# Kernel optimization log

Hardware: AMD Instinct MI355X
Metric: run time of the kernel (lower is better)

The kernel has to match this reference:

```python
import jax, jax.numpy as jnp
import numpy as np

B, S, HID, NH = 8, 1024, 1024, 16
HD = HID // NH  # 64
STR = 128
NEG = -1e10


def setup_inputs() -> dict:
    key = jax.random.key(0)
    ks = jax.random.split(key, 16)
    def lin(k, fan_in, fan_out):
        bound = 1.0 / np.sqrt(fan_in)
        kw, kb = jax.random.split(k)
        W = jax.random.uniform(kw, (fan_in, fan_out), jnp.float32, -bound, bound)
        b = jax.random.uniform(kb, (fan_out,), jnp.float32, -bound, bound)
        return W, b
    Wq, bq = lin(ks[0], HID, HID)
    Wk, bk = lin(ks[1], HID, HID)
    Wv, bv = lin(ks[2], HID, HID)
    Wsk, bsk = lin(ks[3], HID, STR)
    Wsv, bsv = lin(ks[4], HID, STR)
    Wo, bo = lin(ks[5], HID + STR, HID)
    return {
        "query": jax.random.normal(ks[6], (B, S, HID), jnp.float32),
        "key": jax.random.normal(ks[7], (B, S, HID), jnp.float32),
        "value": jax.random.normal(ks[8], (B, S, HID), jnp.float32),
        "x_rsa": jax.random.normal(ks[9], (B, S, STR), jnp.float32),
        "mask": jax.random.randint(ks[10], (B, 1, 1, S), 0, 2, jnp.int32),
        "rsa_mask": jax.random.randint(ks[11], (B, 1, 1, S), 0, 2, jnp.int32),
        "Wq": Wq, "bq": bq, "Wk": Wk, "bk": bk, "Wv": Wv, "bv": bv,
        "Wsk": Wsk, "bsk": bsk, "Wsv": Wsv, "bsv": bsv, "Wo": Wo, "bo": bo,
    }


def reference(query, key, value, x_rsa, mask, rsa_mask,
              Wq, bq, Wk, bk, Wv, bv, Wsk, bsk, Wsv, bsv, Wo, bo):
    scale = jnp.sqrt(jnp.float32(HD))
    Q = (query @ Wq + bq).reshape(B, S, NH, HD).transpose(0, 2, 1, 3)   # [B,NH,S,HD]
    K = (key @ Wk + bk).reshape(B, S, NH, HD).transpose(0, 2, 1, 3)
    V = (value @ Wv + bv).reshape(B, S, NH, HD).transpose(0, 2, 1, 3)
    str_K = (key @ Wsk + bsk)[:, None, :, :]    # [B,1,S,128]
    str_V = (value @ Wsv + bsv)[:, None, :, :]
    rsa_Q = x_rsa[:, None, :, :]                # [B,1,S,128]

    energy = jnp.einsum('bhqd,bhkd->bhqk', Q, K)           # [B,NH,S,S]
    rsa_energy = jnp.einsum('bhqd,bhkd->bhqk', rsa_Q, str_K)  # [B,1,S,S]
    # torch order: mask first, then divide by scale
    energy = jnp.where(mask == 0, NEG, energy) / scale
    rsa_energy = jnp.where(mask == 0, NEG, rsa_energy)
    rsa_energy = jnp.where(rsa_mask == 0, NEG, rsa_energy)  # str_scale == 1

    attention = jax.nn.softmax(energy, axis=-1)
    rsa_attention = jax.nn.softmax(rsa_energy, axis=-1)
    # dropout is identity in eval mode
    x = jnp.einsum('bhqk,bhkd->bhqd', attention, V)          # [B,NH,S,HD]
    rsa_x = jnp.einsum('bhqk,bhkd->bhqd', rsa_attention, str_V)  # [B,1,S,128]
    x = x.transpose(0, 2, 1, 3).reshape(B, S, HID)
    rsa_x = rsa_x.transpose(0, 2, 1, 3).reshape(B, S, STR)
    out = jnp.concatenate((x, rsa_x), axis=-1) @ Wo + bo     # [B,S,HID]
    return out, attention, rsa_attention
```

## Files before the change

kernel.cpp:

```cpp
#include <hip/hip_runtime.h>
#include <stdint.h>

typedef unsigned int u32;
typedef _Float16 f16_t;

typedef _Float16 f16x8 __attribute__((ext_vector_type(8)));
typedef __fp16   fp16x2 __attribute__((ext_vector_type(2)));
typedef float    f32x4 __attribute__((ext_vector_type(4)));

__device__ __forceinline__ f32x4 mfma16(f16x8 a, f16x8 b, f32x4 c){
  return __builtin_amdgcn_mfma_f32_16x16x32_f16(a, b, c, 0, 0, 0);
}
__device__ __forceinline__ float fexp2(float x){ return __builtin_amdgcn_exp2f(x); }
__device__ __forceinline__ u32 pkrtz(float a, float b){
  union { fp16x2 h; u32 u; } cv; cv.h = __builtin_amdgcn_cvt_pkrtz(a, b); return cv.u;
}

template<int N>
__device__ __forceinline__ void barrier_vmleave(){
  asm volatile("s_waitcnt vmcnt(%0)" :: "i"(N) : "memory");
  __builtin_amdgcn_s_barrier();
}

__device__ __forceinline__ void gl_lds16(const void* g, void* l){
  typedef const __attribute__((address_space(1))) void* gasp;
  typedef __attribute__((address_space(3))) void* lasp;
  gasp gp = reinterpret_cast<gasp>(reinterpret_cast<uintptr_t>(g));
  lasp lp = reinterpret_cast<lasp>(static_cast<u32>(reinterpret_cast<uintptr_t>(l)));
  __builtin_amdgcn_global_load_lds(gp, lp, 16, 0, 0);
}

template<int NBYTES, int ROWB, int NT>
__device__ __forceinline__ void stage_swz(const char* gbase, u32 gstrideB, char* lds, int tid){
  const u32 lane = (u32)(tid & 63);
  #pragma unroll
  for (int j = 0; j < NBYTES/(NT*16); ++j){
    u32 o   = (u32)(j*NT + tid) * 16u;
    u32 row = o / (u32)ROWB;
    u32 col = (o % (u32)ROWB) ^ ((row & ((u32)(ROWB>>4)-1u)) << 4);
    gl_lds16(gbase + (size_t)row * gstrideB + col, lds + (o - lane*16u));
  }
}

template<int ROWB>
__device__ __forceinline__ u32 swzb(u32 row, u32 col){
  return col ^ ((row & ((u32)(ROWB>>4)-1u)) << 4);
}

template<int ROWB>
__device__ __forceinline__ f16x8 frag_ld(const char* lds, u32 row, u32 kbyte){
  return *reinterpret_cast<const f16x8*>(lds + (size_t)row*ROWB + swzb<ROWB>(row, kbyte));
}

__device__ __forceinline__ void cvt8(const float* __restrict__ in, f16_t* __restrict__ out, u32 i){
  const f32x4* p = reinterpret_cast<const f32x4*>(in) + 2*(size_t)i;
  f32x4 a = p[0], b = p[1];
  f16x8 v;
  v[0]=(f16_t)a[0]; v[1]=(f16_t)a[1]; v[2]=(f16_t)a[2]; v[3]=(f16_t)a[3];
  v[4]=(f16_t)b[0]; v[5]=(f16_t)b[1]; v[6]=(f16_t)b[2]; v[7]=(f16_t)b[3];
  *(reinterpret_cast<f16x8*>(out) + i) = v;
}

__global__ void prep_all(const float* __restrict__ q, const float* __restrict__ k,
                         const float* __restrict__ v, const float* __restrict__ xr,
                         const int* __restrict__ mask, const int* __restrict__ rmask,
                         f16_t* __restrict__ qo, f16_t* __restrict__ ko,
                         f16_t* __restrict__ vo, f16_t* __restrict__ xo,
                         float* __restrict__ mb, float* __restrict__ rb,
                         const float* __restrict__ Wq, const float* __restrict__ Wk,
                         const float* __restrict__ Wv, const float* __restrict__ Wsk,
                         const float* __restrict__ Wsv, const float* __restrict__ Wo,
                         f16_t* __restrict__ wqT, f16_t* __restrict__ wkT, f16_t* __restrict__ wvT,
                         f16_t* __restrict__ wskT, f16_t* __restrict__ wsvT, f16_t* __restrict__ woT)
{
  __shared__ float tile[32][33];
  u32 b = blockIdx.x;
  if (b < 12288u){
    const float* in; f16_t* out; u32 base;
    if (b < 4096u){ in=q; out=qo; base=0u; }
    else if (b < 8192u){ in=k; out=ko; base=4096u; }
    else { in=v; out=vo; base=8192u; }
    cvt8(in, out, (b-base)*256u + threadIdx.x);
  } else if (b < 12800u){
    cvt8(xr, xo, (b-12288u)*256u + threadIdx.x);
  } else if (b < 12832u){
    u32 i = (b-12800u)*256u + threadIdx.x;
    int m = mask[i]; int r = rmask[i];
    mb[i] = m ? 0.0f : -1.0e9f;
    rb[i] = (m && r) ? 0.0f : -1.0e9f;
  } else {
    u32 t = b - 12832u;
    const float* W; f16_t* WT; u32 K, N, i, j;
    if (t < 3072u){
      u32 w = t >> 10, l = t & 1023u;
      W = w==0 ? Wq : w==1 ? Wk : Wv;
      WT = w==0 ? wqT : w==1 ? wkT : wvT;
      K = 1024u; N = 1024u; i = l & 31u; j = l >> 5;
    } else if (t < 3328u){
      u32 l = t - 3072u;
      W  = l < 128u ? Wsk : Wsv;
      WT = l < 128u ? wskT : wsvT;
      l &= 127u;
      K = 1024u; N = 128u; i = l & 31u; j = l >> 5;
    } else {
      u32 l = t - 3328u;
      W = Wo; WT = woT; K = 1152u; N = 1024u; i = l % 36u; j = l / 36u;
    }
    const u32 k0 = i*32u, n0 = j*32u;
    const int tt = threadIdx.x;
    const int r = tt >> 3, c4 = (tt & 7) * 4;
    f32x4 val = *reinterpret_cast<const f32x4*>(W + (size_t)(k0 + r)*N + n0 + c4);
    tile[r][c4+0]=val[0]; tile[r][c4+1]=val[1]; tile[r][c4+2]=val[2]; tile[r][c4+3]=val[3];
    __syncthreads();
    union { f16_t x[4]; uint64_t u; } pk;
    #pragma unroll
    for (int jj=0;jj<4;++jj) pk.x[jj] = (f16_t)tile[c4+jj][r];
    *reinterpret_cast<uint64_t*>(WT + (size_t)(n0 + r)*K + k0 + c4) = pk.u;
  }
}

struct GArg { const f16_t* A; const f16_t* Bt; const float* bias; void* C; u32 lda, ldb, ldc, K; int mode; };
struct GPack { GArg g[5]; int single; };

__global__ __launch_bounds__(256, 2)
void gemm_bt(GPack p)
{
  __shared__ char As[2][16384];
  __shared__ char Bs[2][16384];
  GArg g; u32 bn;
  const u32 bm = blockIdx.y * 128u;
  if (p.single >= 0){ g = p.g[p.single]; bn = blockIdx.x*128u; }
  else if (blockIdx.z == 0u){ if (blockIdx.x >= 2u) return; g = p.g[3u+blockIdx.x]; bn = 0u; }
  else { g = p.g[blockIdx.z-1u]; bn = blockIdx.x*128u; }

  const int tid = threadIdx.x, lane = tid & 63, wid = tid >> 6;
  const int wr = wid >> 1, wc = wid & 1;
  const char* Ab = (const char*)(g.A + (size_t)bm * g.lda);
  const char* Bb = (const char*)(g.Bt + (size_t)bn * g.ldb);
  const u32 ldaB = g.lda*2u, ldbB = g.ldb*2u;
  const bool swp = (g.mode != 2);

  f32x4 acc[4][4] = {};
  const int nt = (int)(g.K >> 6);

  stage_swz<16384,128,256>(Ab, ldaB, As[0], tid);
  stage_swz<16384,128,256>(Bb, ldbB, Bs[0], tid);
  __syncthreads();

  for (int t = 0; t < nt; ++t){
    if (t + 1 < nt){
      stage_swz<16384,128,256>(Ab + (size_t)(t+1)*128, ldaB, As[(t+1)&1], tid);
      stage_swz<16384,128,256>(Bb + (size_t)(t+1)*128, ldbB, Bs[(t+1)&1], tid);
    }
    const char* as = As[t&1]; const char* bs = Bs[t&1];
    f16x8 af[4][2], bf[4][2];
    #pragma unroll
    for (int mi=0; mi<4; ++mi)
      #pragma unroll
      for (int ks=0; ks<2; ++ks)
        af[mi][ks] = frag_ld<128>(as, (u32)(wr*64 + mi*16 + (lane&15)), (u32)(ks*64 + ((lane>>4)<<4)));
    #pragma unroll
    for (int ni=0; ni<4; ++ni)
      #pragma unroll
      for (int ks=0; ks<2; ++ks)
        bf[ni][ks] = frag_ld<128>(bs, (u32)(wc*64 + ni*16 + (lane&15)), (u32)(ks*64 + ((lane>>4)<<4)));
    if (swp){
      #pragma unroll
      for (int mi=0; mi<4; ++mi)
        #pragma unroll
        for (int ni=0; ni<4; ++ni)
          #pragma unroll
          for (int ks=0; ks<2; ++ks)
            acc[mi][ni] = mfma16(bf[ni][ks], af[mi][ks], acc[mi][ni]);
    } else {
      #pragma unroll
      for (int mi=0; mi<4; ++mi)
        #pragma unroll
        for (int ni=0; ni<4; ++ni)
          #pragma unroll
          for (int ks=0; ks<2; ++ks)
            acc[mi][ni] = mfma16(af[mi][ks], bf[ni][ks], acc[mi][ni]);
    }
    __syncthreads();
  }

  if (g.mode == 2){
    float bv[4];
    #pragma unroll
    for (int ni=0; ni<4; ++ni) bv[ni] = g.bias[bn + wc*64 + ni*16 + (lane&15)];
    f16_t* C = (f16_t*)g.C;
    #pragma unroll
    for (int mi=0; mi<4; ++mi){
      #pragma unroll
      for (int ni=0; ni<4; ++ni){
        u32 n  = bn + (u32)(wc*64 + ni*16 + (lane&15));
        u32 m0 = bm + (u32)(wr*64 + mi*16 + ((lane>>4)<<2));
        size_t idx0 = ((size_t)(m0>>10)*g.ldc + n)*1024 + (m0 & 1023);
        union { f16_t v[4]; uint64_t u; } pk;
        #pragma unroll
        for (int r=0;r<4;++r) pk.v[r] = (f16_t)(acc[mi][ni][r] + bv[ni]);
        *reinterpret_cast<uint64_t*>(C + idx0) = pk.u;
      }
    }
  } else {
    f32x4 bf4[4];
    #pragma unroll
    for (int ni=0; ni<4; ++ni)
      bf4[ni] = *reinterpret_cast<const f32x4*>(g.bias + bn + wc*64 + ni*16 + ((lane>>4)<<2));
    #pragma unroll
    for (int mi=0; mi<4; ++mi){
      u32 m = bm + (u32)(wr*64 + mi*16 + (lane&15));
      #pragma unroll
      for (int ni=0; ni<4; ++ni){
        u32 n0 = bn + (u32)(wc*64 + ni*16 + ((lane>>4)<<2));
        if (g.mode == 0){
          float* C = (float*)g.C;
          f32x4 v = acc[mi][ni] + bf4[ni];
          *reinterpret_cast<f32x4*>(C + (size_t)m*g.ldc + n0) = v;
        } else if (g.mode == 1){
          f16_t* C = (f16_t*)g.C;
          size_t idx = (((size_t)(m>>10)*16 + (n0>>6))*1024 + (m&1023))*64 + (n0&63);
          union { f16_t v[4]; uint64_t u; } pk;
          #pragma unroll
          for (int r=0;r<4;++r) pk.v[r] = (f16_t)(acc[mi][ni][r] + bf4[ni][r]);
          *reinterpret_cast<uint64_t*>(C + idx) = pk.u;
        } else {
          f16_t* C = (f16_t*)g.C;
          union { f16_t v[4]; uint64_t u; } pk;
          #pragma unroll
          for (int r=0;r<4;++r) pk.v[r] = (f16_t)(acc[mi][ni][r] + bf4[ni][r]);
          *reinterpret_cast<uint64_t*>(C + (size_t)m*g.ldc + n0) = pk.u;
        }
      }
    }
  }
}

template<int D, int KCH, int BSHIFT, int SCALEBIT>
__device__ __forceinline__ void attn_fused_body(char* smem,
    const f16_t* __restrict__ Qg, const f16_t* __restrict__ Kg, const f16_t* __restrict__ Vtg,
    const float* __restrict__ mbias,
    float* __restrict__ attnOut, f16_t* __restrict__ xout, u32 xld, u32 xcolAdd,
    const int tid, const u32 qt, const u32 batch)
{
  constexpr int S = 1024;
  constexpr int ROWB  = D*2;
  constexpr int ROWBV = KCH*2;
  constexpr int MI   = KCH/16;
  constexpr int KSL  = D/32;
  constexpr int PSL  = KCH/32;
  constexpr int MIPV = D/16;
  char* Qs  = smem;
  char* Ks0 = Qs + 128*ROWB;
  char* Ks1 = Ks0 + KCH*ROWB;
  char* Vs0 = Ks1 + KCH*ROWB;
  char* Vs1 = Vs0 + D*ROWBV;

  const int lane = tid & 63, wq = tid >> 6;
  const int ql = lane & 15, h = lane >> 4;
  const u32 bb = batch >> BSHIFT;
  const float scale = SCALEBIT ? 0.1803368801111244f : 1.4426950408889634f;
  const f16_t* qb = Qg + ((size_t)batch*S + (size_t)qt*128)*D;
  const f16_t* kb = Kg + (size_t)batch*S*D;
  const char* vtb = (const char*)(Vtg + (size_t)batch*D*S);
  const float* mbb = mbias + (size_t)bb*S;

  const u32 q = qt*128u + (u32)(wq*16 + ql);
  float* arow = attnOut + (size_t)batch*S*S + (size_t)q*S;

  constexpr int NCH = S / KCH;

  stage_swz<128*ROWB, ROWB, 512>((const char*)qb, ROWB, Qs, tid);
  stage_swz<KCH*ROWB, ROWB, 512>((const char*)kb, ROWB, Ks0, tid);
  __syncthreads();

  float sacc = 0.0f;
  for (int ch = 0; ch < NCH; ++ch){
    if (ch + 1 < NCH)
      stage_swz<KCH*ROWB, ROWB, 512>((const char*)(kb + (size_t)(ch+1)*KCH*D), ROWB, ((ch+1)&1)?Ks1:Ks0, tid);
    const char* ks = (ch&1) ? Ks1 : Ks0;

    f32x4 acc[MI] = {};
    #pragma unroll
    for (int ksl=0; ksl<KSL; ++ksl){
      f16x8 bf = frag_ld<ROWB>(Qs, (u32)(wq*16 + ql), (u32)(ksl*64 + h*16));
      #pragma unroll
      for (int mi=0; mi<MI; ++mi){
        f16x8 af = frag_ld<ROWB>(ks, (u32)(mi*16 + ql), (u32)(ksl*64 + h*16));
        acc[mi] = mfma16(af, bf, acc[mi]);
      }
    }
    #pragma unroll
    for (int mi=0; mi<MI; ++mi){
      f32x4 mb = *reinterpret_cast<const f32x4*>(mbb + ch*KCH + mi*16 + h*4);
      #pragma unroll
      for (int r=0;r<4;++r) sacc += fexp2(acc[mi][r]*scale + mb[r]);
    }
    __syncthreads();
  }

  sacc += __shfl_xor(sacc, 16);
  sacc += __shfl_xor(sacc, 32);
  const float rreg = 1.0f / sacc;

  f32x4 accX[MIPV] = {};
  stage_swz<KCH*ROWB, ROWB, 512>((const char*)kb, ROWB, Ks0, tid);
  stage_swz<D*ROWBV, ROWBV, 512>(vtb, (u32)(S*2), Vs0, tid);
  __syncthreads();

  const int bidx = ((ql | ((h & 1) << 5)) << 2);

  for (int ch = 0; ch < NCH; ++ch){
    if (ch + 1 < NCH){
      stage_swz<KCH*ROWB, ROWB, 512>((const char*)(kb + (size_t)(ch+1)*KCH*D), ROWB, ((ch+1)&1)?Ks1:Ks0, tid);
      stage_swz<D*ROWBV, ROWBV, 512>(vtb + (size_t)(ch+1)*KCH*2, (u32)(S*2), ((ch+1)&1)?Vs1:Vs0, tid);
    }
    const char* ks = (ch&1) ? Ks1 : Ks0;
    const char* vs = (ch&1) ? Vs1 : Vs0;

    f32x4 acc[MI] = {};
    #pragma unroll
    for (int ksl=0; ksl<KSL; ++ksl){
      f16x8 bf = frag_ld<ROWB>(Qs, (u32)(wq*16 + ql), (u32)(ksl*64 + h*16));
      #pragma unroll
      for (int mi=0; mi<MI; ++mi){
        f16x8 af = frag_ld<ROWB>(ks, (u32)(mi*16 + ql), (u32)(ksl*64 + h*16));
        acc[mi] = mfma16(af, bf, acc[mi]);
      }
    }

    u32 pk[MI][2];
    #pragma unroll
    for (int mi=0; mi<MI; ++mi){
      f32x4 mb = *reinterpret_cast<const f32x4*>(mbb + ch*KCH + mi*16 + h*4);
      f32x4 pv;
      #pragma unroll
      for (int r=0;r<4;++r)
        pv[r] = fexp2(acc[mi][r]*scale + mb[r]) * rreg;
      *reinterpret_cast<f32x4*>(arow + ch*KCH + mi*16 + h*4) = pv;
      pk[mi][0] = pkrtz(pv[0], pv[1]);
      pk[mi][1] = pkrtz(pv[2], pv[3]);
    }

    #pragma unroll
    for (int psl=0; psl<PSL; ++psl){
      union { u32 w[4]; f16x8 v; } pb;
      #pragma unroll
      for (int s=0; s<4; ++s){
        int ii = bidx + ((s & 2) ? 64 : 0);
        u32 pa  = (u32)__builtin_amdgcn_ds_bpermute(ii, (int)pk[2*psl][s&1]);
        u32 pbv = (u32)__builtin_amdgcn_ds_bpermute(ii, (int)pk[2*psl+1][s&1]);
        pb.w[s] = (lane & 32) ? pbv : pa;
      }
      #pragma unroll
      for (int mi2=0; mi2<MIPV; ++mi2){
        f16x8 vf = frag_ld<ROWBV>(vs, (u32)(mi2*16 + ql), (u32)(psl*64 + h*16));
        accX[mi2] = mfma16(vf, pb.v, accX[mi2]);
      }
    }

    barrier_vmleave<MI>();
  }

  u32 col0 = (batch & ((1u<<BSHIFT)-1u)) * (u32)D + xcolAdd;
  #pragma unroll
  for (int mi2=0; mi2<MIPV; ++mi2){
    union { f16_t v[4]; uint64_t u; } pk4;
    #pragma unroll
    for (int r=0;r<4;++r) pk4.v[r] = (f16_t)accX[mi2][r];
    *reinterpret_cast<uint64_t*>(xout + ((size_t)bb*S + q)*xld + col0 + mi2*16 + h*4) = pk4.u;
  }
}

__global__ __launch_bounds__(512, 4)
void attn_all(const f16_t* __restrict__ Qh, const f16_t* __restrict__ Kh,
              const f16_t* __restrict__ Vth, const float* __restrict__ mbias,
              float* __restrict__ attnp,
              const f16_t* __restrict__ xrf, const f16_t* __restrict__ strK,
              const f16_t* __restrict__ strVt, const float* __restrict__ rbias,
              float* __restrict__ rsap,
              f16_t* __restrict__ conc)
{
  __shared__ char smem[65536];
  const int tid = threadIdx.x;
  const u32 qt = blockIdx.y & 7u;
  const u32 bh = blockIdx.x * 17u + (blockIdx.y >> 3);
  if (bh < 8u) attn_fused_body<128,32,0,0>(smem, xrf, strK, strVt, rbias, rsap, conc, 1152u, 1024u, tid, qt, bh);
  else         attn_fused_body<64, 64,4,1>(smem, Qh,  Kh,   Vth,   mbias, attnp, conc, 1152u, 0u,    tid, qt, bh-8u);
}

extern "C" void kernel_launch(void* const* d_in, const int* in_sizes, int n_in,
                              void* d_out, int out_size, void* d_ws, size_t ws_size,
                              hipStream_t stream)
{
  const float* query = (const float*)d_in[0];
  const float* key   = (const float*)d_in[1];
  const float* value = (const float*)d_in[2];
  const float* x_rsa = (const float*)d_in[3];
  const int*   mask  = (const int*)d_in[4];
  const int*   rmask = (const int*)d_in[5];
  const float* Wq = (const float*)d_in[6];  const float* bq = (const float*)d_in[7];
  const float* Wk = (const float*)d_in[8];  const float* bk = (const float*)d_in[9];
  const float* Wv = (const float*)d_in[10]; const float* bv = (const float*)d_in[11];
  const float* Wsk= (const float*)d_in[12]; const float* bsk= (const float*)d_in[13];
  const float* Wsv= (const float*)d_in[14]; const float* bsv= (const float*)d_in[15];
  const float* Wo = (const float*)d_in[16]; const float* bo = (const float*)d_in[17];

  char* ws = (char*)d_ws;
  size_t off = 0;
  auto alloc = [&](size_t bytes)->char*{ char* p = ws + off; off += (bytes + 255) & ~(size_t)255; return p; };

  f16_t* q16  = (f16_t*)alloc(16777216);
  f16_t* k16  = (f16_t*)alloc(16777216);
  f16_t* v16  = (f16_t*)alloc(16777216);
  f16_t* xrf  = (f16_t*)alloc(2097152);
  f16_t* wqT  = (f16_t*)alloc(2097152);
  f16_t* wkT  = (f16_t*)alloc(2097152);
  f16_t* wvT  = (f16_t*)alloc(2097152);
  f16_t* wskT = (f16_t*)alloc(262144);
  f16_t* wsvT = (f16_t*)alloc(262144);
  f16_t* woT  = (f16_t*)alloc(2359296);
  f16_t* Qh   = (f16_t*)alloc(16777216);
  f16_t* Kh   = (f16_t*)alloc(16777216);
  f16_t* Vth  = (f16_t*)alloc(16777216);
  f16_t* strK = (f16_t*)alloc(2097152);
  f16_t* strVt= (f16_t*)alloc(2097152);
  f16_t* conc = (f16_t*)alloc(18874368);
  float* mbias= (float*)alloc(32768);
  float* rbias= (float*)alloc(32768);

  prep_all<<<17312,256,0,stream>>>(query, key, value, x_rsa, mask, rmask,
                                   q16, k16, v16, xrf, mbias, rbias,
                                   Wq, Wk, Wv, Wsk, Wsv, Wo,
                                   wqT, wkT, wvT, wskT, wsvT, woT);

  {
    GPack pm{};
    pm.g[0] = {q16, wqT,  bq,  (void*)Qh,    1024u,1024u,0u,   1024u, 1};
    pm.g[1] = {k16, wkT,  bk,  (void*)Kh,    1024u,1024u,0u,   1024u, 1};
    pm.g[2] = {v16, wvT,  bv,  (void*)Vth,   1024u,1024u,1024u,1024u, 2};
    pm.g[3] = {k16, wskT, bsk, (void*)strK,  1024u,1024u,128u, 1024u, 3};
    pm.g[4] = {v16, wsvT, bsv, (void*)strVt, 1024u,1024u,128u, 1024u, 2};
    pm.single = -1;
    gemm_bt<<<dim3(8,64,4),256,0,stream>>>(pm);
  }

  float* outp  = (float*)d_out;
  float* attnp = outp + 8388608;
  float* rsap  = outp + 8388608 + 134217728;

  attn_all<<<dim3(8,136),512,0,stream>>>(Qh, Kh, Vth, mbias, attnp,
                                         xrf, strK, strVt, rbias, rsap, conc);

  {
    GPack po{};
    po.g[0] = {conc, woT, bo, (void*)outp, 1152u,1152u,1024u,1152u, 0};
    po.g[1] = po.g[0]; po.g[2] = po.g[0]; po.g[3] = po.g[0]; po.g[4] = po.g[0];
    po.single = 0;
    gemm_bt<<<dim3(8,64,1),256,0,stream>>>(po);
  }

  (void)in_sizes; (void)n_in; (void)out_size; (void)ws_size;
}
```

Measured before the change: 401.5 us.

## Stage softmax probabilities in LDS for coalesced attention stores and MFMA operands

Each wave packs its fp16 softmax probabilities into a new swizzled LDS buffer. The P·V MFMA now reads its B operand from that buffer instead of rebuilding it with ds_bpermute shuffles. The fp32 attention output is written from the same buffer in a row-contiguous layout, four threads per row, replacing scattered per-lane stores. The goal is better coalescing of the dominant attention-matrix write and fewer cross-lane permutes. The cost is an extra 8KB of shared memory, and the stored attention probabilities are now fp16-rounded before conversion back to fp32.

Result: slower. 410.2 us (+2.2%).

```diff
diff --git a/kernel.cpp b/kernel.cpp
--- a/kernel.cpp
+++ b/kernel.cpp
@@ -246,6 +246,7 @@
   constexpr int S = 1024;
   constexpr int ROWB  = D*2;
   constexpr int ROWBV = KCH*2;
+  constexpr int PROWB = KCH*2;
   constexpr int MI   = KCH/16;
   constexpr int KSL  = D/32;
   constexpr int PSL  = KCH/32;
@@ -255,6 +256,7 @@
   char* Ks1 = Ks0 + KCH*ROWB;
   char* Vs0 = Ks1 + KCH*ROWB;
   char* Vs1 = Vs0 + D*ROWBV;
+  char* pout = Vs1 + D*ROWBV;
 
   const int lane = tid & 63, wq = tid >> 6;
   const int ql = lane & 15, h = lane >> 4;
@@ -266,7 +268,7 @@
   const float* mbb = mbias + (size_t)bb*S;
 
   const u32 q = qt*128u + (u32)(wq*16 + ql);
-  float* arow = attnOut + (size_t)batch*S*S + (size_t)q*S;
+  const u32 qrow = (u32)(wq*16 + ql);
 
   constexpr int NCH = S / KCH;
 
@@ -283,7 +285,7 @@
     f32x4 acc[MI] = {};
     #pragma unroll
     for (int ksl=0; ksl<KSL; ++ksl){
-      f16x8 bf = frag_ld<ROWB>(Qs, (u32)(wq*16 + ql), (u32)(ksl*64 + h*16));
+      f16x8 bf = frag_ld<ROWB>(Qs, qrow, (u32)(ksl*64 + h*16));
       #pragma unroll
       for (int mi=0; mi<MI; ++mi){
         f16x8 af = frag_ld<ROWB>(ks, (u32)(mi*16 + ql), (u32)(ksl*64 + h*16));
@@ -308,8 +310,6 @@
   stage_swz<D*ROWBV, ROWBV, 512>(vtb, (u32)(S*2), Vs0, tid);
   __syncthreads();
 
-  const int bidx = ((ql | ((h & 1) << 5)) << 2);
-
   for (int ch = 0; ch < NCH; ++ch){
     if (ch + 1 < NCH){
       stage_swz<KCH*ROWB, ROWB, 512>((const char*)(kb + (size_t)(ch+1)*KCH*D), ROWB, ((ch+1)&1)?Ks1:Ks0, tid);
@@ -321,7 +321,7 @@
     f32x4 acc[MI] = {};
     #pragma unroll
     for (int ksl=0; ksl<KSL; ++ksl){
-      f16x8 bf = frag_ld<ROWB>(Qs, (u32)(wq*16 + ql), (u32)(ksl*64 + h*16));
+      f16x8 bf = frag_ld<ROWB>(Qs, qrow, (u32)(ksl*64 + h*16));
       #pragma unroll
       for (int mi=0; mi<MI; ++mi){
         f16x8 af = frag_ld<ROWB>(ks, (u32)(mi*16 + ql), (u32)(ksl*64 + h*16));
@@ -329,7 +329,6 @@
       }
     }
 
-    u32 pk[MI][2];
     #pragma unroll
     for (int mi=0; mi<MI; ++mi){
       f32x4 mb = *reinterpret_cast<const f32x4*>(mbb + ch*KCH + mi*16 + h*4);
@@ -337,25 +336,35 @@
       #pragma unroll
       for (int r=0;r<4;++r)
         pv[r] = fexp2(acc[mi][r]*scale + mb[r]) * rreg;
-      *reinterpret_cast<f32x4*>(arow + ch*KCH + mi*16 + h*4) = pv;
-      pk[mi][0] = pkrtz(pv[0], pv[1]);
-      pk[mi][1] = pkrtz(pv[2], pv[3]);
+      union { u32 w[2]; uint64_t u; } pq;
+      pq.w[0] = pkrtz(pv[0], pv[1]);
+      pq.w[1] = pkrtz(pv[2], pv[3]);
+      u32 colb = (u32)(mi*32 + h*8);
+      *reinterpret_cast<uint64_t*>(pout + (size_t)qrow*PROWB + swzb<PROWB>(qrow, colb)) = pq.u;
     }
 
     #pragma unroll
     for (int psl=0; psl<PSL; ++psl){
-      union { u32 w[4]; f16x8 v; } pb;
-      #pragma unroll
-      for (int s=0; s<4; ++s){
-        int ii = bidx + ((s & 2) ? 64 : 0);
-        u32 pa  = (u32)__builtin_amdgcn_ds_bpermute(ii, (int)pk[2*psl][s&1]);
-        u32 pbv = (u32)__builtin_amdgcn_ds_bpermute(ii, (int)pk[2*psl+1][s&1]);
-        pb.w[s] = (lane & 32) ? pbv : pa;
-      }
+      f16x8 pf = frag_ld<PROWB>(pout, qrow, (u32)(psl*64 + h*16));
       #pragma unroll
       for (int mi2=0; mi2<MIPV; ++mi2){
         f16x8 vf = frag_ld<ROWBV>(vs, (u32)(mi2*16 + ql), (u32)(psl*64 + h*16));
-        accX[mi2] = mfma16(vf, pb.v, accX[mi2]);
+        accX[mi2] = mfma16(vf, pf, accX[mi2]);
+      }
+    }
+
+    {
+      const u32 q2 = (u32)tid >> 2;
+      float* arow2 = attnOut + (size_t)batch*S*S + ((size_t)qt*128 + q2)*S + (size_t)ch*KCH;
+      #pragma unroll
+      for (int j=0; j<MI; ++j){
+        u32 colb = (u32)(tid&3)*8u + (u32)j*32u;
+        union { f16_t v[4]; uint64_t u; } rd;
+        rd.u = *reinterpret_cast<const uint64_t*>(pout + (size_t)q2*PROWB + swzb<PROWB>(q2, colb));
+        f32x4 w;
+        #pragma unroll
+        for (int r=0;r<4;++r) w[r] = (float)rd.v[r];
+        *reinterpret_cast<f32x4*>(arow2 + (colb>>1)) = w;
       }
     }
 
@@ -381,7 +390,7 @@
               float* __restrict__ rsap,
               f16_t* __restrict__ conc)
 {
-  __shared__ char smem[65536];
+  __shared__ char smem[73728];
   const int tid = threadIdx.x;
   const u32 qt = blockIdx.y & 7u;
   const u32 bh = blockIdx.x * 17u + (blockIdx.y >> 3);
```
